# Kernel optimization log

Measured on AMD Instinct MI355X. Metric: run time of the kernel, lower is better.

## Reference

```python
import jax, jax.numpy as jnp
import numpy as np


def log_g(x):
    # log of g(x) = x + 0.5 if x >= 0 else sigmoid(x)  (minGRU paper Appendix B)
    return jnp.where(x >= 0, jnp.log(jax.nn.relu(x) + 0.5), -jax.nn.softplus(-x))


def parallel_scan_log(log_coeffs, log_values):
    # log_coeffs: [B, T, H]; log_values: [B, T+1, H]
    a_star = jnp.pad(jnp.cumsum(log_coeffs, axis=1), ((0, 0), (1, 0), (0, 0)))  # [B, T+1, H]
    log_h = a_star + jax.lax.cumlogsumexp(log_values - a_star, axis=1)
    return jnp.exp(log_h)  # [B, T+1, H]


def setup_inputs() -> dict:
    key = jax.random.key(0)
    ks = jax.random.split(key, 6)
    B, T, D, H = 4, 4096, 1024, 1024
    scale = 1.0 / np.sqrt(D)
    return {
        "x": jax.random.normal(ks[0], (B, T, D), dtype=jnp.float32),
        "h_0": jax.random.uniform(ks[1], (B, H), dtype=jnp.float32),
        "Wz": jax.random.normal(ks[2], (H, D), dtype=jnp.float32) * scale,
        "bz": jnp.zeros((H,), dtype=jnp.float32),
        "Wh": jax.random.normal(ks[3], (H, D), dtype=jnp.float32) * scale,
        "bh": jnp.zeros((H,), dtype=jnp.float32),
    }


def reference(x, h_0, Wz, bz, Wh, bh):
    T = x.shape[1]
    k = jnp.einsum("btd,hd->bth", x, Wz) + bz          # linear_z(x)
    log_z = -jax.nn.softplus(-k)                          # log sigmoid(k)
    log_coeffs = -jax.nn.softplus(k)                      # log (1 - sigmoid(k))
    log_h_0 = log_g(h_0)[:, None, :]                      # [B, 1, H]
    log_tilde_h = log_g(jnp.einsum("btd,hd->bth", x, Wh) + bh)
    log_values = jnp.concatenate([log_h_0, log_z + log_tilde_h], axis=1)  # [B, T+1, H]
    h = parallel_scan_log(log_coeffs, log_values)
    return h[:, -T:, :]
```

## Files before the change

kernel.cpp:

```cpp
#include <hip/hip_runtime.h>
#include <hip/hip_bf16.h>
#include <hip/hip_fp16.h>

#define B_ 4
#define T_ 4096
#define D_ 1024
#define H_ 1024
#define M_ (B_ * T_)

typedef __attribute__((ext_vector_type(8))) short short8;
typedef __attribute__((ext_vector_type(4))) float f32x4;

__device__ __forceinline__ unsigned short f2bf(float f) {
    unsigned int u = __float_as_uint(f);
    u += 0x7fffu + ((u >> 16) & 1u);
    return (unsigned short)(u >> 16);
}

__global__ __launch_bounds__(256) void convert_all(
    const float* __restrict__ x, const float* __restrict__ wz, const float* __restrict__ wh,
    unsigned short* __restrict__ xbp, unsigned short* __restrict__ wcbp)
{
    int i = blockIdx.x * 256 + threadIdx.x;
    const float* srcrow;
    unsigned short* dst;
    if (i < 2097152) {
        int l = i & 63, s = i >> 6;
        int c = s & 31, r = s >> 5;
        int row = r * 16 + (l & 15);
        int k   = c * 32 + (l >> 4) * 8;
        srcrow = x + (size_t)row * D_ + k;
        dst = xbp + ((size_t)(c * 1024 + r) * 64 + l) * 8;
    } else {
        int j = i - 2097152;
        int l = j & 63, s = j >> 6;
        int c = s & 31, r = s >> 5;
        int ir = r * 16 + (l & 15);
        int a = ir >> 5, wi = ir & 31;
        const float* m = (wi < 16) ? wz : wh;
        int srow = a * 16 + (wi & 15);
        int k = c * 32 + (l >> 4) * 8;
        srcrow = m + (size_t)srow * D_ + k;
        dst = wcbp + ((size_t)(c * 128 + r) * 64 + l) * 8;
    }
    float4 f0 = ((const float4*)srcrow)[0];
    float4 f1 = ((const float4*)srcrow)[1];
    ushort4 u0, u1;
    u0.x = f2bf(f0.x); u0.y = f2bf(f0.y); u0.z = f2bf(f0.z); u0.w = f2bf(f0.w);
    u1.x = f2bf(f1.x); u1.y = f2bf(f1.y); u1.z = f2bf(f1.z); u1.w = f2bf(f1.w);
    ((ushort4*)dst)[0] = u0;
    ((ushort4*)dst)[1] = u1;
}

__global__ __launch_bounds__(256, 2) void dual_gemm_kernel(
    const unsigned short* __restrict__ xbp,
    const unsigned short* __restrict__ wcbp,
    const float* __restrict__ bz,
    const float* __restrict__ bh,
    __half2* __restrict__ av16,
    float2* __restrict__ chunkAV)
{
    const int tid  = threadIdx.x;
    const int lane = tid & 63;
    const int w    = __builtin_amdgcn_readfirstlane(tid >> 6);
    const int r16  = lane & 15;
    const int q    = lane >> 4;

    const int bid = blockIdx.x;
    const int swz = (bid & 7) * 128 + (bid >> 3);
    const int nbg = swz & 7;
    const int mbw = swz >> 3;
    const int nbw = nbg * 4 + w;

    const unsigned short* gA = xbp  + (size_t)(mbw * 8) * 512 + lane * 8;
    const unsigned short* gB = wcbp + (size_t)(nbw * 4) * 512 + lane * 8;

#define LOADK(FA, FB, c) do { \
    const unsigned short* _a = gA + (size_t)(c) * 524288; \
    const unsigned short* _b = gB + (size_t)(c) * 65536; \
    _Pragma("unroll") \
    for (int m = 0; m < 8; ++m) FA[m] = *(const short8*)(_a + m * 512); \
    _Pragma("unroll") \
    for (int n = 0; n < 4; ++n) FB[n] = *(const short8*)(_b + n * 512); \
} while (0)

#define MFMA32(FA, FB) do { \
    __builtin_amdgcn_s_setprio(1); \
    _Pragma("unroll") \
    for (int m = 0; m < 8; ++m) \
        _Pragma("unroll") \
        for (int n = 0; n < 4; ++n) \
            acc[m][n] = __builtin_amdgcn_mfma_f32_16x16x32_bf16(FA[m], FB[n], acc[m][n], 0, 0, 0); \
    __builtin_amdgcn_s_setprio(0); \
} while (0)

    f32x4 acc[8][4] = {};
    short8 fa0[8], fb0[4], fa1[8], fb1[4];

    LOADK(fa0, fb0, 0);
    for (int cc = 0; cc < 32; cc += 2) {
        LOADK(fa1, fb1, cc + 1);
        MFMA32(fa0, fb0);
        if (cc < 30) LOADK(fa0, fb0, cc + 2);
        MFMA32(fa1, fb1);
    }

    const int mrow0 = mbw * 128;
    const int ncol0 = nbw * 32 + r16;
    const float bzv0 = bz[ncol0],      bhv0 = bh[ncol0];
    const float bzv1 = bz[ncol0 + 16], bhv1 = bh[ncol0 + 16];
#pragma unroll
    for (int hh = 0; hh < 2; ++hh) {
        float CA0 = 1.0f, CV0 = 0.0f, CA1 = 1.0f, CV1 = 0.0f;
#pragma unroll
        for (int mm = 0; mm < 4; ++mm) {
            const int mf = hh * 4 + mm;
            float LA0 = 1.0f, LV0 = 0.0f, LA1 = 1.0f, LV1 = 0.0f;
#pragma unroll
            for (int rr = 0; rr < 4; ++rr) {
                const size_t m = (size_t)(mrow0 + mf * 16 + q * 4 + rr);
                {
                    float kv = acc[mf][0][rr] + bzv0;
                    float hv = acc[mf][1][rr] + bhv0;
                    float tk = __expf(-fabsf(kv));
                    float ik = 1.0f / (1.0f + tk);
                    float sig = (kv >= 0.0f) ? ik : tk * ik;
                    float ac  = (kv >= 0.0f) ? tk * ik : ik;
                    float th = __expf(-fabsf(hv));
                    float ih = 1.0f / (1.0f + th);
                    float gh = (hv >= 0.0f) ? (hv + 0.5f) : th * ih;
                    float vv = sig * gh;
                    av16[m * H_ + ncol0] = __floats2half2_rn(ac, vv);
                    LV0 = ac * LV0 + vv;
                    LA0 = ac * LA0;
                }
                {
                    float kv = acc[mf][2][rr] + bzv1;
                    float hv = acc[mf][3][rr] + bhv1;
                    float tk = __expf(-fabsf(kv));
                    float ik = 1.0f / (1.0f + tk);
                    float sig = (kv >= 0.0f) ? ik : tk * ik;
                    float ac  = (kv >= 0.0f) ? tk * ik : ik;
                    float th = __expf(-fabsf(hv));
                    float ih = 1.0f / (1.0f + th);
                    float gh = (hv >= 0.0f) ? (hv + 0.5f) : th * ih;
                    float vv = sig * gh;
                    av16[m * H_ + ncol0 + 16] = __floats2half2_rn(ac, vv);
                    LV1 = ac * LV1 + vv;
                    LA1 = ac * LA1;
                }
            }
#pragma unroll
            for (int mask = 16; mask <= 32; mask <<= 1) {
                float PA0 = __shfl_xor(LA0, mask);
                float PV0 = __shfl_xor(LV0, mask);
                float PA1 = __shfl_xor(LA1, mask);
                float PV1 = __shfl_xor(LV1, mask);
                if (lane & mask) {
                    LV0 = LA0 * PV0 + LV0; LA0 = LA0 * PA0;
                    LV1 = LA1 * PV1 + LV1; LA1 = LA1 * PA1;
                } else {
                    LV0 = PA0 * LV0 + PV0; LA0 = PA0 * LA0;
                    LV1 = PA1 * LV1 + PV1; LA1 = PA1 * LA1;
                }
            }
            CV0 = LA0 * CV0 + LV0; CA0 = LA0 * CA0;
            CV1 = LA1 * CV1 + LV1; CA1 = LA1 * CA1;
        }
        if (q == 0) {
            const int cglob = mbw * 2 + hh;
            const int base = (cglob & 63) * 4096 + (cglob >> 6) * 1024;
            chunkAV[base + ncol0]      = make_float2(CA0, CV0);
            chunkAV[base + ncol0 + 16] = make_float2(CA1, CV1);
        }
    }
#undef LOADK
#undef MFMA32
}

__global__ __launch_bounds__(256) void scan_pass3(const __half2* __restrict__ av16,
                                                  const float2* __restrict__ chunkAV,
                                                  const float* __restrict__ h0,
                                                  float* __restrict__ out) {
    int g = blockIdx.x * blockDim.x + threadIdx.x;
    int n = g & (H_ - 1);
    int rest = g >> 10;
    int c = rest & 63;
    int b = rest >> 6;
    float x = h0[b * H_ + n];
    float h;
    if (x >= 0.0f) { h = x + 0.5f; }
    else { float t = __expf(x); h = t / (1.0f + t); }
    for (int cc = 0; cc < c; ++cc) {
        float2 s = chunkAV[cc * 4096 + b * 1024 + n];
        h = s.x * h + s.y;
    }
    const __half2* base = av16 + ((size_t)(b * T_ + c * 64)) * H_ + n;
    float* obase = out + ((size_t)(b * T_ + c * 64)) * H_ + n;
#pragma unroll 8
    for (int t = 0; t < 64; ++t) {
        float2 p = __half22float2(base[(size_t)t * H_]);
        h = p.x * h + p.y;
        obase[(size_t)t * H_] = h;
    }
}

extern "C" void kernel_launch(void* const* d_in, const int* in_sizes, int n_in,
                              void* d_out, int out_size, void* d_ws, size_t ws_size,
                              hipStream_t stream) {
    const float* x  = (const float*)d_in[0];
    const float* h0 = (const float*)d_in[1];
    const float* Wz = (const float*)d_in[2];
    const float* bz = (const float*)d_in[3];
    const float* Wh = (const float*)d_in[4];
    const float* bh = (const float*)d_in[5];
    float* out = (float*)d_out;

    char* ws = (char*)d_ws;
    unsigned short* xbp  = (unsigned short*)(ws);
    unsigned short* wcbp = (unsigned short*)(ws + 33554432);
    __half2* av16        = (__half2*)(ws + 37748736);
    float2* chunkAV      = (float2*)(ws + 104857600);

    convert_all<<<9216, 256, 0, stream>>>(x, Wz, Wh, xbp, wcbp);

    dual_gemm_kernel<<<1024, 256, 0, stream>>>(xbp, wcbp, bz, bh, av16, chunkAV);

    scan_pass3<<<1024, 256, 0, stream>>>(av16, chunkAV, h0, out);
}
```

Measured before the change: 236.7 us.

## Fuse scan into GEMM epilogue with decoupled-lookback chained carry propagation

After: 720.4 us. 204% more time.

```diff
diff --git a/kernel.cpp b/kernel.cpp
--- a/kernel.cpp
+++ b/kernel.cpp
@@ -52,13 +52,15 @@
     ((ushort4*)dst)[1] = u1;
 }
 
-__global__ __launch_bounds__(256, 2) void dual_gemm_kernel(
+__global__ __launch_bounds__(256, 2) void gemm_scan_kernel(
     const unsigned short* __restrict__ xbp,
     const unsigned short* __restrict__ wcbp,
     const float* __restrict__ bz,
     const float* __restrict__ bh,
-    __half2* __restrict__ av16,
-    float2* __restrict__ chunkAV)
+    const float* __restrict__ h0,
+    float* __restrict__ hpub,
+    int* __restrict__ flags,
+    float* __restrict__ out)
 {
     const int tid  = threadIdx.x;
     const int lane = tid & 63;
@@ -67,10 +69,10 @@
     const int q    = lane >> 4;
 
     const int bid = blockIdx.x;
-    const int swz = (bid & 7) * 128 + (bid >> 3);
-    const int nbg = swz & 7;
-    const int mbw = swz >> 3;
+    const int nbg = bid >> 7;
+    const int mbw = bid & 127;
     const int nbw = nbg * 4 + w;
+    const int b   = mbw >> 5;
 
     const unsigned short* gA = xbp  + (size_t)(mbw * 8) * 512 + lane * 8;
     const unsigned short* gB = wcbp + (size_t)(nbw * 4) * 512 + lane * 8;
@@ -109,6 +111,9 @@
     const int ncol0 = nbw * 32 + r16;
     const float bzv0 = bz[ncol0],      bhv0 = bh[ncol0];
     const float bzv1 = bz[ncol0 + 16], bhv1 = bh[ncol0 + 16];
+
+    __half2 av[64];
+    float CAh[2][2], CVh[2][2];
 #pragma unroll
     for (int hh = 0; hh < 2; ++hh) {
         float CA0 = 1.0f, CV0 = 0.0f, CA1 = 1.0f, CV1 = 0.0f;
@@ -118,7 +123,6 @@
             float LA0 = 1.0f, LV0 = 0.0f, LA1 = 1.0f, LV1 = 0.0f;
 #pragma unroll
             for (int rr = 0; rr < 4; ++rr) {
-                const size_t m = (size_t)(mrow0 + mf * 16 + q * 4 + rr);
                 {
                     float kv = acc[mf][0][rr] + bzv0;
                     float hv = acc[mf][1][rr] + bhv0;
@@ -130,7 +134,7 @@
                     float ih = 1.0f / (1.0f + th);
                     float gh = (hv >= 0.0f) ? (hv + 0.5f) : th * ih;
                     float vv = sig * gh;
-                    av16[m * H_ + ncol0] = __floats2half2_rn(ac, vv);
+                    av[(0 * 2 + hh) * 16 + mm * 4 + rr] = __floats2half2_rn(ac, vv);
                     LV0 = ac * LV0 + vv;
                     LA0 = ac * LA0;
                 }
@@ -145,7 +149,7 @@
                     float ih = 1.0f / (1.0f + th);
                     float gh = (hv >= 0.0f) ? (hv + 0.5f) : th * ih;
                     float vv = sig * gh;
-                    av16[m * H_ + ncol0 + 16] = __floats2half2_rn(ac, vv);
+                    av[(1 * 2 + hh) * 16 + mm * 4 + rr] = __floats2half2_rn(ac, vv);
                     LV1 = ac * LV1 + vv;
                     LA1 = ac * LA1;
                 }
@@ -167,42 +171,73 @@
             CV0 = LA0 * CV0 + LV0; CA0 = LA0 * CA0;
             CV1 = LA1 * CV1 + LV1; CA1 = LA1 * CA1;
         }
-        if (q == 0) {
-            const int cglob = mbw * 2 + hh;
-            const int base = (cglob & 63) * 4096 + (cglob >> 6) * 1024;
-            chunkAV[base + ncol0]      = make_float2(CA0, CV0);
-            chunkAV[base + ncol0 + 16] = make_float2(CA1, CV1);
+        CAh[hh][0] = CA0; CVh[hh][0] = CV0;
+        CAh[hh][1] = CA1; CVh[hh][1] = CV1;
+    }
+
+    float hin0, hin1;
+    if ((mbw & 31) == 0) {
+        float x0 = h0[b * H_ + ncol0];
+        float x1 = h0[b * H_ + ncol0 + 16];
+        if (x0 >= 0.0f) hin0 = x0 + 0.5f;
+        else { float t = __expf(x0); hin0 = t / (1.0f + t); }
+        if (x1 >= 0.0f) hin1 = x1 + 0.5f;
+        else { float t = __expf(x1); hin1 = t / (1.0f + t); }
+    } else {
+        if (tid == 0) {
+            while (__hip_atomic_load(&flags[bid - 1], __ATOMIC_ACQUIRE,
+                                     __HIP_MEMORY_SCOPE_AGENT) == 0)
+                __builtin_amdgcn_s_sleep(8);
+        }
+        __syncthreads();
+        hin0 = __hip_atomic_load(&hpub[(mbw - 1) * 1024 + ncol0],
+                                 __ATOMIC_RELAXED, __HIP_MEMORY_SCOPE_AGENT);
+        hin1 = __hip_atomic_load(&hpub[(mbw - 1) * 1024 + ncol0 + 16],
+                                 __ATOMIC_RELAXED, __HIP_MEMORY_SCOPE_AGENT);
+    }
+    const float e10 = CAh[0][0] * hin0 + CVh[0][0];
+    const float e11 = CAh[0][1] * hin1 + CVh[0][1];
+    const float ho0 = CAh[1][0] * e10 + CVh[1][0];
+    const float ho1 = CAh[1][1] * e11 + CVh[1][1];
+    if (q == 0) {
+        __hip_atomic_store(&hpub[mbw * 1024 + ncol0], ho0,
+                           __ATOMIC_RELAXED, __HIP_MEMORY_SCOPE_AGENT);
+        __hip_atomic_store(&hpub[mbw * 1024 + ncol0 + 16], ho1,
+                           __ATOMIC_RELAXED, __HIP_MEMORY_SCOPE_AGENT);
+    }
+    __syncthreads();
+    if (tid == 0) {
+        __threadfence();
+        __hip_atomic_store(&flags[bid], 1, __ATOMIC_RELEASE,
+                           __HIP_MEMORY_SCOPE_AGENT);
+    }
+
+#pragma unroll
+    for (int hh = 0; hh < 2; ++hh) {
+#pragma unroll
+        for (int gg = 0; gg < 2; ++gg) {
+            float h = (hh == 0) ? (gg == 0 ? hin0 : hin1)
+                                : (gg == 0 ? e10 : e11);
+            const int ncol = ncol0 + gg * 16;
+#pragma unroll
+            for (int mm = 0; mm < 4; ++mm) {
+#pragma unroll
+                for (int qt = 0; qt < 4; ++qt) {
+                    if (q == qt) {
+#pragma unroll
+                        for (int rr = 0; rr < 4; ++rr) {
+                            float2 p = __half22float2(av[(gg * 2 + hh) * 16 + mm * 4 + rr]);
+                            h = p.x * h + p.y;
+                            out[(size_t)(mrow0 + (hh * 4 + mm) * 16 + qt * 4 + rr) * H_ + ncol] = h;
+                        }
+                    }
+                    h = __shfl(h, qt * 16 + r16);
+                }
+            }
         }
     }
 #undef LOADK
 #undef MFMA32
-}
-
-__global__ __launch_bounds__(256) void scan_pass3(const __half2* __restrict__ av16,
-                                                  const float2* __restrict__ chunkAV,
-                                                  const float* __restrict__ h0,
-                                                  float* __restrict__ out) {
-    int g = blockIdx.x * blockDim.x + threadIdx.x;
-    int n = g & (H_ - 1);
-    int rest = g >> 10;
-    int c = rest & 63;
-    int b = rest >> 6;
-    float x = h0[b * H_ + n];
-    float h;
-    if (x >= 0.0f) { h = x + 0.5f; }
-    else { float t = __expf(x); h = t / (1.0f + t); }
-    for (int cc = 0; cc < c; ++cc) {
-        float2 s = chunkAV[cc * 4096 + b * 1024 + n];
-        h = s.x * h + s.y;
-    }
-    const __half2* base = av16 + ((size_t)(b * T_ + c * 64)) * H_ + n;
-    float* obase = out + ((size_t)(b * T_ + c * 64)) * H_ + n;
-#pragma unroll 8
-    for (int t = 0; t < 64; ++t) {
-        float2 p = __half22float2(base[(size_t)t * H_]);
-        h = p.x * h + p.y;
-        obase[(size_t)t * H_] = h;
-    }
 }
 
 extern "C" void kernel_launch(void* const* d_in, const int* in_sizes, int n_in,
@@ -219,12 +254,13 @@
     char* ws = (char*)d_ws;
     unsigned short* xbp  = (unsigned short*)(ws);
     unsigned short* wcbp = (unsigned short*)(ws + 33554432);
-    __half2* av16        = (__half2*)(ws + 37748736);
-    float2* chunkAV      = (float2*)(ws + 104857600);
+    float* hpub          = (float*)(ws + 37748736);
+    int*   flags         = (int*)(ws + 38273024);
+
+    hipMemsetAsync(flags, 0, 1024 * sizeof(int), stream);
 
     convert_all<<<9216, 256, 0, stream>>>(x, Wz, Wh, xbp, wcbp);
 
-    dual_gemm_kernel<<<1024, 256, 0, stream>>>(xbp, wcbp, bz, bh, av16, chunkAV);
-
-    scan_pass3<<<1024, 256, 0, stream>>>(av16, chunkAV, h0, out);
-}
+    gemm_scan_kernel<<<1024, 256, 0, stream>>>(xbp, wcbp, bz, bh, h0,
+                                               hpub, flags, out);
+}
```
